# Kernel tuning notes

Measured on AMD Instinct MI355X. Metric: run time of the kernel, lower is better.

## Reference

```python
import jax, jax.numpy as jnp
import numpy as np

N_HEAD = 16
EMBED = 1024
HEAD_DIM = EMBED // N_HEAD  # 64
HALF = HEAD_DIM // 2        # 32
T = 2048                    # total packed tokens
NSEG = 4
SEG = T // NSEG             # 512 tokens per packed sequence
SCALE = HEAD_DIM ** -0.5


def _apply_rotary_vision(t, freqs):
    # t: [T, H, D], freqs: [T, D/2] -> Qwen2-VL style vision RoPE
    cos = jnp.concatenate([jnp.cos(freqs), jnp.cos(freqs)], axis=-1)[:, None, :]  # [T,1,D]
    sin = jnp.concatenate([jnp.sin(freqs), jnp.sin(freqs)], axis=-1)[:, None, :]
    t1, t2 = t[..., :HALF], t[..., HALF:]
    rot = jnp.concatenate([-t2, t1], axis=-1)  # rotate_half
    return t * cos + rot * sin


def setup_inputs() -> dict:
    key = jax.random.key(0)
    k1, k2, k3, k4, k5 = jax.random.split(key, 5)
    hidden_states = jax.random.normal(k1, (T, EMBED), dtype=jnp.float32)
    cu_seqlens = (jnp.arange(NSEG + 1, dtype=jnp.int32) * SEG)  # [0,512,...,2048]
    # realistic rotary freqs: position within each segment * inverse frequencies
    pos = jnp.tile(jnp.arange(SEG, dtype=jnp.float32), NSEG)  # [T]
    inv_freq = 1.0 / (10000.0 ** (jnp.arange(HALF, dtype=jnp.float32) / HALF))
    rotary_pos_emb = pos[:, None] * inv_freq[None, :]  # [T, HALF]
    std = 0.02
    wq = jax.random.normal(k2, (EMBED, EMBED), dtype=jnp.float32) * std
    wk = jax.random.normal(k3, (EMBED, EMBED), dtype=jnp.float32) * std
    wv = jax.random.normal(k4, (EMBED, EMBED), dtype=jnp.float32) * std
    wo = jax.random.normal(k5, (EMBED, EMBED), dtype=jnp.float32) * std
    return {"hidden_states": hidden_states, "cu_seqlens": cu_seqlens,
            "rotary_pos_emb": rotary_pos_emb, "wq": wq, "wk": wk, "wv": wv, "wo": wo}


def reference(hidden_states, cu_seqlens, rotary_pos_emb, wq, wk, wv, wo):
    # QKV projections (nn.Linear, bias=False): y = x @ W.T
    q = (hidden_states @ wq.T).reshape(T, N_HEAD, HEAD_DIM)
    k = (hidden_states @ wk.T).reshape(T, N_HEAD, HEAD_DIM)
    v = (hidden_states @ wv.T).reshape(T, N_HEAD, HEAD_DIM)
    q = _apply_rotary_vision(q, rotary_pos_emb)
    k = _apply_rotary_vision(k, rotary_pos_emb)
    # varlen (block-diagonal, non-causal) attention over packed segments
    seg_id = jnp.searchsorted(cu_seqlens, jnp.arange(T, dtype=cu_seqlens.dtype), side='right')
    same_seg = seg_id[:, None] == seg_id[None, :]  # [T, T]
    scores = jnp.einsum('thd,shd->hts', q, k) * SCALE  # [H, T, T]
    scores = jnp.where(same_seg[None, :, :], scores, jnp.finfo(scores.dtype).min)
    probs = jax.nn.softmax(scores, axis=-1)
    attn = jnp.einsum('hts,shd->thd', probs, v).reshape(T, EMBED)
    return attn @ wo.T
```

## Files before the change

kernel.cpp:

```cpp
#include <hip/hip_runtime.h>
#include <cstdint>

#define T_TOK 2048
#define EMBED 1024
#define NH    16
#define HD    64
#define HALF  32
#define SEG   512
#define SL    (0.125f * 1.44269504088896f)

typedef __attribute__((ext_vector_type(8))) __bf16 bf16x8;
typedef __attribute__((ext_vector_type(4))) float  f32x4;
typedef unsigned short u16;
typedef unsigned int   u32;

__device__ __forceinline__ u16 f2bf(float f) {
  u32 u = __builtin_bit_cast(u32, f);
  u += 0x7fffu + ((u >> 16) & 1u);
  return (u16)(u >> 16);
}

__device__ __forceinline__ void gld_lds16(const void* g, void* l) {
  __builtin_amdgcn_global_load_lds(
      reinterpret_cast<__attribute__((address_space(1))) u32*>(
          reinterpret_cast<uintptr_t>(g)),
      reinterpret_cast<__attribute__((address_space(3))) u32*>(
          reinterpret_cast<uintptr_t>(l)),
      16, 0, 0);
}

__global__ __launch_bounds__(256) void convert_k(
    const float* __restrict__ H,  const float* __restrict__ wq,
    const float* __restrict__ wk, const float* __restrict__ wv,
    const float* __restrict__ wo, u16* __restrict__ dst) {
  const size_t gid = (size_t)blockIdx.x * 256 + threadIdx.x;
  const size_t e = gid * 4;
  const float* src; size_t off;
  const size_t HN = (size_t)T_TOK * EMBED;
  if (e < HN) { src = H; off = e; }
  else {
    size_t r = e - HN;
    int w = (int)(r >> 20);
    off = r & ((1u << 20) - 1);
    src = (w == 0) ? wq : (w == 1) ? wk : (w == 2) ? wv : wo;
  }
  const float4 v = *(const float4*)(src + off);
  ushort4 o;
  o.x = f2bf(v.x); o.y = f2bf(v.y); o.z = f2bf(v.z); o.w = f2bf(v.w);
  *(ushort4*)(dst + e) = o;
}

__global__ __launch_bounds__(256) void qkv_k(
    const u16* __restrict__ Hb, const u16* __restrict__ Wb,
    const float* __restrict__ rope, u16* __restrict__ Qb,
    u16* __restrict__ Khh, u16* __restrict__ Vss) {
  constexpr int K = 1024, N = 1024;
  __shared__ alignas(16) u16 As[2][2][128 * 32];
  __shared__ alignas(16) u16 Bs[2][2][128 * 32];
  const int tid = threadIdx.x;
  const int wave = tid >> 6, lane = tid & 63;
  const int quad = lane >> 4, l16 = lane & 15;
  const int bm = blockIdx.y * 128, bn = blockIdx.x * 128;
  const int z = blockIdx.z;
  const u16* Bz = Wb + ((size_t)z << 20);
  const int wm = (wave >> 1) * 64, wn = (wave & 1) * 64;

  f32x4 acc[4][4];
#pragma unroll
  for (int i = 0; i < 4; ++i)
#pragma unroll
    for (int j = 0; j < 4; ++j) { f32x4 zz = {0.f, 0.f, 0.f, 0.f}; acc[i][j] = zz; }

  const int srow = tid >> 2, scol = (tid & 3) * 8;
  const u16* gA = Hb + (size_t)(bm + srow) * K + scol;
  const u16* gB = Bz + (size_t)(bn + srow) * K + scol;

#pragma unroll
  for (int p = 0; p < 2; ++p)
#pragma unroll
    for (int hrow = 0; hrow < 2; ++hrow) {
      gld_lds16(gA + (size_t)hrow * 64 * K + p * 32,
                (char*)&As[0][p][0] + hrow * 4096 + wave * 1024);
      gld_lds16(gB + (size_t)hrow * 64 * K + p * 32,
                (char*)&Bs[0][p][0] + hrow * 4096 + wave * 1024);
    }

  for (int kk = 0; kk < K; kk += 64) {
    __syncthreads();
    const int cur = (kk >> 6) & 1, nxt = cur ^ 1;
    if (kk + 64 < K) {
      const int kn = kk + 64;
#pragma unroll
      for (int p = 0; p < 2; ++p)
#pragma unroll
        for (int hrow = 0; hrow < 2; ++hrow) {
          gld_lds16(gA + (size_t)hrow * 64 * K + kn + p * 32,
                    (char*)&As[nxt][p][0] + hrow * 4096 + wave * 1024);
          gld_lds16(gB + (size_t)hrow * 64 * K + kn + p * 32,
                    (char*)&Bs[nxt][p][0] + hrow * 4096 + wave * 1024);
        }
    }
#pragma unroll
    for (int p = 0; p < 2; ++p) {
      const u16* Ac = &As[cur][p][0];
      const u16* Bc = &Bs[cur][p][0];
      bf16x8 af[4], bfv[4];
#pragma unroll
      for (int i = 0; i < 4; ++i)
        af[i] = *(const bf16x8*)(Ac + (wm + i * 16 + l16) * 32 + quad * 8);
#pragma unroll
      for (int j = 0; j < 4; ++j)
        bfv[j] = *(const bf16x8*)(Bc + (wn + j * 16 + l16) * 32 + quad * 8);
#pragma unroll
      for (int i = 0; i < 4; ++i)
#pragma unroll
        for (int j = 0; j < 4; ++j)
          acc[i][j] = __builtin_amdgcn_mfma_f32_16x16x32_bf16(af[i], bfv[j],
                                                              acc[i][j], 0, 0, 0);
    }
  }

  const int h = (bn + wn) >> 6;
  if (z == 0) {
#pragma unroll
    for (int i = 0; i < 4; ++i)
#pragma unroll
      for (int r = 0; r < 4; ++r) {
        const int t = bm + wm + i * 16 + quad * 4 + r;
        const float f0 = rope[t * HALF + l16];
        const float f1 = rope[t * HALF + 16 + l16];
        float s0, c0, s1, c1;
        __sincosf(f0, &s0, &c0);
        __sincosf(f1, &s1, &c1);
        const float v0 = acc[i][0][r], v1 = acc[i][1][r];
        const float v2 = acc[i][2][r], v3 = acc[i][3][r];
        const size_t base = (size_t)t * N + bn + wn + l16;
        Qb[base]      = f2bf(v0 * c0 - v2 * s0);
        Qb[base + 16] = f2bf(v1 * c1 - v3 * s1);
        Qb[base + 32] = f2bf(v2 * c0 + v0 * s0);
        Qb[base + 48] = f2bf(v3 * c1 + v1 * s1);
      }
  } else if (z == 1) {
#pragma unroll
    for (int i = 0; i < 4; ++i)
#pragma unroll
      for (int r = 0; r < 4; ++r) {
        const int t = bm + wm + i * 16 + quad * 4 + r;
        const float f0 = rope[t * HALF + l16];
        const float f1 = rope[t * HALF + 16 + l16];
        float s0, c0, s1, c1;
        __sincosf(f0, &s0, &c0);
        __sincosf(f1, &s1, &c1);
        const float v0 = acc[i][0][r], v1 = acc[i][1][r];
        const float v2 = acc[i][2][r], v3 = acc[i][3][r];
        const size_t b0 = ((size_t)(h * 2 + 0) * T_TOK + t) * 32;
        const size_t b1 = ((size_t)(h * 2 + 1) * T_TOK + t) * 32;
        Khh[b0 + l16]      = f2bf(v0 * c0 - v2 * s0);
        Khh[b0 + 16 + l16] = f2bf(v1 * c1 - v3 * s1);
        Khh[b1 + l16]      = f2bf(v2 * c0 + v0 * s0);
        Khh[b1 + 16 + l16] = f2bf(v3 * c1 + v1 * s1);
      }
  } else {
#pragma unroll
    for (int i = 0; i < 4; ++i) {
      const int t0 = bm + wm + i * 16 + quad * 4;
      const int tp = t0 >> 5, toff = t0 & 31;
#pragma unroll
      for (int j = 0; j < 4; ++j) {
        const int d = j * 16 + l16;
        ushort4 pk;
        pk.x = f2bf(acc[i][j][0]); pk.y = f2bf(acc[i][j][1]);
        pk.z = f2bf(acc[i][j][2]); pk.w = f2bf(acc[i][j][3]);
        *(ushort4*)(Vss + ((size_t)(h * 64 + tp) * 64 + d) * 32 + toff) = pk;
      }
    }
  }
}

__global__ __launch_bounds__(512) void attn_st(
    const u16* __restrict__ Qb, const u16* __restrict__ Khh,
    const u16* __restrict__ Vss, u16* __restrict__ Ab) {
  const int b = blockIdx.x;
  const int qt = b & 3, seg = (b >> 2) & 3, h = b >> 4;
  const int tid = threadIdx.x;
  const int wave = tid >> 6, lane = tid & 63;
  const int quad = lane >> 4, l16 = lane & 15;

  __shared__ alignas(16) u16 Ks[2][2][64 * 32];
  __shared__ alignas(16) u16 Vs[2][2][64 * 32];

  const int qbase = seg * SEG + qt * 128 + wave * 16;
  const u16* qp = Qb + (size_t)(qbase + l16) * EMBED + h * HD + quad * 8;
  const bf16x8 qf0 = *(const bf16x8*)qp;
  const bf16x8 qf1 = *(const bf16x8*)(qp + 32);

  const u16* Ksrc0 = Khh + ((size_t)(h * 2 + 0) * T_TOK + seg * SEG) * 32;
  const u16* Ksrc1 = Khh + ((size_t)(h * 2 + 1) * T_TOK + seg * SEG) * 32;
  const u16* Vsrc  = Vss + ((size_t)(h * 64 + seg * 16) * 64) * 32;

  float plsum = 0.f;
  f32x4 O[4];
#pragma unroll
  for (int nt = 0; nt < 4; ++nt) { f32x4 z = {0.f, 0.f, 0.f, 0.f}; O[nt] = z; }

  const int toff = tid * 4;
  const int rb = 8 * (l16 >> 2) + (l16 & 3);

  uint2 kreg0 = *(const uint2*)(Ksrc0 + toff);
  uint2 kreg1 = *(const uint2*)(Ksrc1 + toff);
  uint2 vreg0 = *(const uint2*)(Vsrc + toff);
  uint2 vreg1 = *(const uint2*)(Vsrc + 2048 + toff);
  *(uint2*)((char*)&Ks[0][0][0] + tid * 8) = kreg0;
  *(uint2*)((char*)&Ks[0][1][0] + tid * 8) = kreg1;
  *(uint2*)((char*)&Vs[0][0][0] + tid * 8) = vreg0;
  *(uint2*)((char*)&Vs[0][1][0] + tid * 8) = vreg1;
  kreg0 = *(const uint2*)(Ksrc0 + 2048 + toff);
  kreg1 = *(const uint2*)(Ksrc1 + 2048 + toff);
  vreg0 = *(const uint2*)(Vsrc + 4096 + toff);
  vreg1 = *(const uint2*)(Vsrc + 4096 + 2048 + toff);
  asm volatile("s_waitcnt lgkmcnt(0)" ::: "memory");
  __builtin_amdgcn_s_barrier();
  __builtin_amdgcn_sched_barrier(0);

  int cur = 0;
  for (int cc = 0; cc < 8; ++cc) {
    f32x4 S[4];
    __builtin_amdgcn_s_setprio(1);
#pragma unroll
    for (int kt = 0; kt < 4; ++kt) {
      const int pk = rb + 4 * (kt & 1) + 32 * (kt >> 1);
      const bf16x8 k0 = *(const bf16x8*)&Ks[cur][0][pk * 32 + quad * 8];
      const bf16x8 k1 = *(const bf16x8*)&Ks[cur][1][pk * 32 + quad * 8];
      f32x4 s = {0.f, 0.f, 0.f, 0.f};
      s = __builtin_amdgcn_mfma_f32_16x16x32_bf16(k0, qf0, s, 0, 0, 0);
      s = __builtin_amdgcn_mfma_f32_16x16x32_bf16(k1, qf1, s, 0, 0, 0);
      S[kt] = s;
    }
    __builtin_amdgcn_s_setprio(0);
    bf16x8 vf0[4], vf1[4];
#pragma unroll
    for (int nt = 0; nt < 4; ++nt) {
      vf0[nt] = *(const bf16x8*)&Vs[cur][0][(nt * 16 + l16) * 32 + quad * 8];
      vf1[nt] = *(const bf16x8*)&Vs[cur][1][(nt * 16 + l16) * 32 + quad * 8];
    }
    u32 lo[4], hi[4];
    float plc = 0.f;
#pragma unroll
    for (int kt = 0; kt < 4; ++kt) {
      const float p0 = exp2f(S[kt][0] * SL), p1 = exp2f(S[kt][1] * SL);
      const float p2 = exp2f(S[kt][2] * SL), p3 = exp2f(S[kt][3] * SL);
      plc += (p0 + p1) + (p2 + p3);
      lo[kt] = (u32)f2bf(p0) | ((u32)f2bf(p1) << 16);
      hi[kt] = (u32)f2bf(p2) | ((u32)f2bf(p3) << 16);
    }
    plsum += plc;
    uint4 w0; w0.x = lo[0]; w0.y = hi[0]; w0.z = lo[1]; w0.w = hi[1];
    uint4 w1; w1.x = lo[2]; w1.y = hi[2]; w1.z = lo[3]; w1.w = hi[3];
    const bf16x8 pf0 = __builtin_bit_cast(bf16x8, w0);
    const bf16x8 pf1 = __builtin_bit_cast(bf16x8, w1);
    __builtin_amdgcn_s_setprio(1);
#pragma unroll
    for (int nt = 0; nt < 4; ++nt) {
      O[nt] = __builtin_amdgcn_mfma_f32_16x16x32_bf16(pf0, vf0[nt], O[nt], 0, 0, 0);
      O[nt] = __builtin_amdgcn_mfma_f32_16x16x32_bf16(pf1, vf1[nt], O[nt], 0, 0, 0);
    }
    __builtin_amdgcn_s_setprio(0);
    if (cc < 7) {
      const int nxt = cur ^ 1;
      *(uint2*)((char*)&Ks[nxt][0][0] + tid * 8) = kreg0;
      *(uint2*)((char*)&Ks[nxt][1][0] + tid * 8) = kreg1;
      *(uint2*)((char*)&Vs[nxt][0][0] + tid * 8) = vreg0;
      *(uint2*)((char*)&Vs[nxt][1][0] + tid * 8) = vreg1;
      if (cc < 6) {
        const size_t kc = (size_t)(cc + 2) * 2048 + toff;
        const size_t vc = (size_t)(cc + 2) * 4096 + toff;
        kreg0 = *(const uint2*)(Ksrc0 + kc);
        kreg1 = *(const uint2*)(Ksrc1 + kc);
        vreg0 = *(const uint2*)(Vsrc + vc);
        vreg1 = *(const uint2*)(Vsrc + vc + 2048);
      }
      asm volatile("s_waitcnt lgkmcnt(0)" ::: "memory");
      __builtin_amdgcn_s_barrier();
      __builtin_amdgcn_sched_barrier(0);
    }
    cur ^= 1;
  }
  plsum += __shfl_xor(plsum, 16);
  plsum += __shfl_xor(plsum, 32);
  float inv[4];
#pragma unroll
  for (int r = 0; r < 4; ++r)
    inv[r] = 1.f / __shfl(plsum, quad * 4 + r);
#pragma unroll
  for (int nt = 0; nt < 4; ++nt)
#pragma unroll
    for (int r = 0; r < 4; ++r) {
      const int trow = qbase + quad * 4 + r;
      Ab[(size_t)trow * EMBED + h * HD + nt * 16 + l16] = f2bf(O[nt][r] * inv[r]);
    }
}

__global__ __launch_bounds__(256) void oproj_k(
    const u16* __restrict__ Ab, const u16* __restrict__ Wo,
    float* __restrict__ out) {
  constexpr int K = 1024, N = 1024;
  __shared__ alignas(16) u16 As[2][2][64 * 32];
  __shared__ alignas(16) u16 Bs[2][2][64 * 32];
  const int tid = threadIdx.x;
  const int wave = tid >> 6, lane = tid & 63;
  const int quad = lane >> 4, l16 = lane & 15;
  const int bm = blockIdx.y * 64, bn = blockIdx.x * 64;

  f32x4 acc[4];
#pragma unroll
  for (int j = 0; j < 4; ++j) { f32x4 z = {0.f, 0.f, 0.f, 0.f}; acc[j] = z; }

  const int srow = tid >> 2, scol = (tid & 3) * 8;
  const u16* gA = Ab + (size_t)(bm + srow) * K + scol;
  const u16* gB = Wo + (size_t)(bn + srow) * K + scol;

#pragma unroll
  for (int p = 0; p < 2; ++p) {
    gld_lds16(gA + p * 32, (char*)&As[0][p][0] + wave * 1024);
    gld_lds16(gB + p * 32, (char*)&Bs[0][p][0] + wave * 1024);
  }

  for (int kk = 0; kk < K; kk += 64) {
    __syncthreads();
    const int cur = (kk >> 6) & 1, nxt = cur ^ 1;
    if (kk + 64 < K) {
      const int kn = kk + 64;
#pragma unroll
      for (int p = 0; p < 2; ++p) {
        gld_lds16(gA + kn + p * 32, (char*)&As[nxt][p][0] + wave * 1024);
        gld_lds16(gB + kn + p * 32, (char*)&Bs[nxt][p][0] + wave * 1024);
      }
    }
#pragma unroll
    for (int p = 0; p < 2; ++p) {
      const u16* Ac = &As[cur][p][0];
      const u16* Bc = &Bs[cur][p][0];
      const bf16x8 af = *(const bf16x8*)(Ac + (wave * 16 + l16) * 32 + quad * 8);
      bf16x8 bfv[4];
#pragma unroll
      for (int j = 0; j < 4; ++j)
        bfv[j] = *(const bf16x8*)(Bc + (j * 16 + l16) * 32 + quad * 8);
#pragma unroll
      for (int j = 0; j < 4; ++j)
        acc[j] = __builtin_amdgcn_mfma_f32_16x16x32_bf16(af, bfv[j],
                                                         acc[j], 0, 0, 0);
    }
  }

#pragma unroll
  for (int r = 0; r < 4; ++r) {
    const int row = bm + wave * 16 + quad * 4 + r;
#pragma unroll
    for (int j = 0; j < 4; ++j)
      out[(size_t)row * N + bn + j * 16 + l16] = acc[j][r];
  }
}

extern "C" void kernel_launch(void* const* d_in, const int* in_sizes, int n_in,
                              void* d_out, int out_size, void* d_ws,
                              size_t ws_size, hipStream_t stream) {
  const float* H    = (const float*)d_in[0];
  const float* rope = (const float*)d_in[2];
  const float* wq   = (const float*)d_in[3];
  const float* wk   = (const float*)d_in[4];
  const float* wv   = (const float*)d_in[5];
  const float* wo   = (const float*)d_in[6];
  float* out        = (float*)d_out;

  constexpr size_t M1 = (size_t)1 << 20;
  if (ws_size < 28 * M1) return;

  u16* ws16 = (u16*)d_ws;
  u16* Hb  = ws16;
  u16* Wb  = ws16 + 2 * M1;
  u16* Qb  = ws16 + 6 * M1;
  u16* Khh = ws16 + 8 * M1;
  u16* Vss = ws16 + 10 * M1;
  u16* Ab  = ws16 + 12 * M1;

  convert_k<<<6144, 256, 0, stream>>>(H, wq, wk, wv, wo, ws16);
  qkv_k<<<dim3(8, 16, 3), 256, 0, stream>>>(Hb, Wb, rope, Qb, Khh, Vss);
  attn_st<<<256, 512, 0, stream>>>(Qb, Khh, Vss, Ab);
  oproj_k<<<dim3(16, 32), 256, 0, stream>>>(Ab, Wb + 3 * M1, out);
}
```

Measured before the change: 123.0 us.

## Fuse Q, K, V projections per head into one block sharing the A tile

```diff
diff --git a/kernel.cpp b/kernel.cpp
--- a/kernel.cpp
+++ b/kernel.cpp
@@ -50,129 +50,109 @@
   *(ushort4*)(dst + e) = o;
 }
 
-__global__ __launch_bounds__(256) void qkv_k(
+__global__ __launch_bounds__(512) void qkv_k(
     const u16* __restrict__ Hb, const u16* __restrict__ Wb,
     const float* __restrict__ rope, u16* __restrict__ Qb,
     u16* __restrict__ Khh, u16* __restrict__ Vss) {
-  constexpr int K = 1024, N = 1024;
+  constexpr int K = 1024;
   __shared__ alignas(16) u16 As[2][2][128 * 32];
-  __shared__ alignas(16) u16 Bs[2][2][128 * 32];
+  __shared__ alignas(16) u16 Bs[3][2][2][64 * 32];
   const int tid = threadIdx.x;
   const int wave = tid >> 6, lane = tid & 63;
   const int quad = lane >> 4, l16 = lane & 15;
-  const int bm = blockIdx.y * 128, bn = blockIdx.x * 128;
-  const int z = blockIdx.z;
-  const u16* Bz = Wb + ((size_t)z << 20);
-  const int wm = (wave >> 1) * 64, wn = (wave & 1) * 64;
-
-  f32x4 acc[4][4];
-#pragma unroll
-  for (int i = 0; i < 4; ++i)
-#pragma unroll
-    for (int j = 0; j < 4; ++j) { f32x4 zz = {0.f, 0.f, 0.f, 0.f}; acc[i][j] = zz; }
-
-  const int srow = tid >> 2, scol = (tid & 3) * 8;
-  const u16* gA = Hb + (size_t)(bm + srow) * K + scol;
-  const u16* gB = Bz + (size_t)(bn + srow) * K + scol;
-
-#pragma unroll
-  for (int p = 0; p < 2; ++p)
-#pragma unroll
-    for (int hrow = 0; hrow < 2; ++hrow) {
-      gld_lds16(gA + (size_t)hrow * 64 * K + p * 32,
-                (char*)&As[0][p][0] + hrow * 4096 + wave * 1024);
-      gld_lds16(gB + (size_t)hrow * 64 * K + p * 32,
-                (char*)&Bs[0][p][0] + hrow * 4096 + wave * 1024);
-    }
+  const int h = blockIdx.x, bm = blockIdx.y * 128;
+  const int bn = h * 64;
+  const int wm = (wave >> 1) * 32, ws = wave & 1;
+
+  f32x4 acc[3][2][2];
+#pragma unroll
+  for (int z = 0; z < 3; ++z)
+#pragma unroll
+    for (int i = 0; i < 2; ++i)
+#pragma unroll
+      for (int j = 0; j < 2; ++j) { f32x4 zz = {0.f, 0.f, 0.f, 0.f}; acc[z][i][j] = zz; }
+
+  const u16* gA = Hb + (size_t)(bm + (tid >> 2)) * K + (tid & 3) * 8;
+  const int brow = (tid >> 2) & 63;
+  const int srow = (brow & 15) + ((brow >> 4) & 1) * 32 + (brow >> 5) * 16;
+  const size_t boff = (size_t)(bn + srow) * K + (tid >> 8) * 32 + (tid & 3) * 8;
+  const u16* gB0 = Wb + ((size_t)0 << 20) + boff;
+  const u16* gB1 = Wb + ((size_t)1 << 20) + boff;
+  const u16* gB2 = Wb + ((size_t)2 << 20) + boff;
+
+#define QKV_STAGE(buf, kkk)                                                   \
+  do {                                                                        \
+    gld_lds16(gA + (kkk),      (char*)&As[buf][0][0] + wave * 1024);          \
+    gld_lds16(gA + (kkk) + 32, (char*)&As[buf][1][0] + wave * 1024);          \
+    gld_lds16(gB0 + (kkk), (char*)&Bs[0][buf][0][0] + wave * 1024);           \
+    gld_lds16(gB1 + (kkk), (char*)&Bs[1][buf][0][0] + wave * 1024);           \
+    gld_lds16(gB2 + (kkk), (char*)&Bs[2][buf][0][0] + wave * 1024);           \
+  } while (0)
+
+  QKV_STAGE(0, 0);
 
   for (int kk = 0; kk < K; kk += 64) {
     __syncthreads();
     const int cur = (kk >> 6) & 1, nxt = cur ^ 1;
-    if (kk + 64 < K) {
-      const int kn = kk + 64;
-#pragma unroll
-      for (int p = 0; p < 2; ++p)
-#pragma unroll
-        for (int hrow = 0; hrow < 2; ++hrow) {
-          gld_lds16(gA + (size_t)hrow * 64 * K + kn + p * 32,
-                    (char*)&As[nxt][p][0] + hrow * 4096 + wave * 1024);
-          gld_lds16(gB + (size_t)hrow * 64 * K + kn + p * 32,
-                    (char*)&Bs[nxt][p][0] + hrow * 4096 + wave * 1024);
-        }
-    }
+    if (kk + 64 < K) QKV_STAGE(nxt, kk + 64);
 #pragma unroll
     for (int p = 0; p < 2; ++p) {
-      const u16* Ac = &As[cur][p][0];
-      const u16* Bc = &Bs[cur][p][0];
-      bf16x8 af[4], bfv[4];
-#pragma unroll
-      for (int i = 0; i < 4; ++i)
-        af[i] = *(const bf16x8*)(Ac + (wm + i * 16 + l16) * 32 + quad * 8);
-#pragma unroll
-      for (int j = 0; j < 4; ++j)
-        bfv[j] = *(const bf16x8*)(Bc + (wn + j * 16 + l16) * 32 + quad * 8);
-#pragma unroll
-      for (int i = 0; i < 4; ++i)
-#pragma unroll
-        for (int j = 0; j < 4; ++j)
-          acc[i][j] = __builtin_amdgcn_mfma_f32_16x16x32_bf16(af[i], bfv[j],
-                                                              acc[i][j], 0, 0, 0);
-    }
-  }
-
-  const int h = (bn + wn) >> 6;
-  if (z == 0) {
-#pragma unroll
-    for (int i = 0; i < 4; ++i)
-#pragma unroll
-      for (int r = 0; r < 4; ++r) {
-        const int t = bm + wm + i * 16 + quad * 4 + r;
-        const float f0 = rope[t * HALF + l16];
-        const float f1 = rope[t * HALF + 16 + l16];
-        float s0, c0, s1, c1;
-        __sincosf(f0, &s0, &c0);
-        __sincosf(f1, &s1, &c1);
-        const float v0 = acc[i][0][r], v1 = acc[i][1][r];
-        const float v2 = acc[i][2][r], v3 = acc[i][3][r];
-        const size_t base = (size_t)t * N + bn + wn + l16;
-        Qb[base]      = f2bf(v0 * c0 - v2 * s0);
-        Qb[base + 16] = f2bf(v1 * c1 - v3 * s1);
-        Qb[base + 32] = f2bf(v2 * c0 + v0 * s0);
-        Qb[base + 48] = f2bf(v3 * c1 + v1 * s1);
+      bf16x8 af[2], bfv[3][2];
+#pragma unroll
+      for (int i = 0; i < 2; ++i)
+        af[i] = *(const bf16x8*)(&As[cur][p][0] + (wm + i * 16 + l16) * 32 + quad * 8);
+#pragma unroll
+      for (int z = 0; z < 3; ++z)
+#pragma unroll
+        for (int j = 0; j < 2; ++j)
+          bfv[z][j] = *(const bf16x8*)(&Bs[z][cur][p][0] +
+                                       (ws * 32 + j * 16 + l16) * 32 + quad * 8);
+#pragma unroll
+      for (int z = 0; z < 3; ++z)
+#pragma unroll
+        for (int i = 0; i < 2; ++i)
+#pragma unroll
+          for (int j = 0; j < 2; ++j)
+            acc[z][i][j] = __builtin_amdgcn_mfma_f32_16x16x32_bf16(
+                af[i], bfv[z][j], acc[z][i][j], 0, 0, 0);
+    }
+  }
+#undef QKV_STAGE
+
+  const int dcol = ws * 16 + l16;
+#pragma unroll
+  for (int i = 0; i < 2; ++i)
+#pragma unroll
+    for (int r = 0; r < 4; ++r) {
+      const int t = bm + wm + i * 16 + quad * 4 + r;
+      const float f = rope[t * HALF + dcol];
+      float s, c;
+      __sincosf(f, &s, &c);
+      {
+        const float v0 = acc[0][i][0][r], v1 = acc[0][i][1][r];
+        const size_t base = (size_t)t * EMBED + bn + dcol;
+        Qb[base]      = f2bf(v0 * c - v1 * s);
+        Qb[base + 32] = f2bf(v1 * c + v0 * s);
       }
-  } else if (z == 1) {
-#pragma unroll
-    for (int i = 0; i < 4; ++i)
-#pragma unroll
-      for (int r = 0; r < 4; ++r) {
-        const int t = bm + wm + i * 16 + quad * 4 + r;
-        const float f0 = rope[t * HALF + l16];
-        const float f1 = rope[t * HALF + 16 + l16];
-        float s0, c0, s1, c1;
-        __sincosf(f0, &s0, &c0);
-        __sincosf(f1, &s1, &c1);
-        const float v0 = acc[i][0][r], v1 = acc[i][1][r];
-        const float v2 = acc[i][2][r], v3 = acc[i][3][r];
+      {
+        const float v0 = acc[1][i][0][r], v1 = acc[1][i][1][r];
         const size_t b0 = ((size_t)(h * 2 + 0) * T_TOK + t) * 32;
         const size_t b1 = ((size_t)(h * 2 + 1) * T_TOK + t) * 32;
-        Khh[b0 + l16]      = f2bf(v0 * c0 - v2 * s0);
-        Khh[b0 + 16 + l16] = f2bf(v1 * c1 - v3 * s1);
-        Khh[b1 + l16]      = f2bf(v2 * c0 + v0 * s0);
-        Khh[b1 + 16 + l16] = f2bf(v3 * c1 + v1 * s1);
+        Khh[b0 + dcol] = f2bf(v0 * c - v1 * s);
+        Khh[b1 + dcol] = f2bf(v1 * c + v0 * s);
       }
-  } else {
-#pragma unroll
-    for (int i = 0; i < 4; ++i) {
-      const int t0 = bm + wm + i * 16 + quad * 4;
-      const int tp = t0 >> 5, toff = t0 & 31;
-#pragma unroll
-      for (int j = 0; j < 4; ++j) {
-        const int d = j * 16 + l16;
-        ushort4 pk;
-        pk.x = f2bf(acc[i][j][0]); pk.y = f2bf(acc[i][j][1]);
-        pk.z = f2bf(acc[i][j][2]); pk.w = f2bf(acc[i][j][3]);
-        *(ushort4*)(Vss + ((size_t)(h * 64 + tp) * 64 + d) * 32 + toff) = pk;
-      }
+    }
+#pragma unroll
+  for (int i = 0; i < 2; ++i) {
+    const int t0 = bm + wm + i * 16 + quad * 4;
+    const int tp = t0 >> 5, toff = t0 & 31;
+#pragma unroll
+    for (int j = 0; j < 2; ++j) {
+      const int d = dcol + j * 32;
+      ushort4 pk;
+      pk.x = f2bf(acc[2][i][j][0]); pk.y = f2bf(acc[2][i][j][1]);
+      pk.z = f2bf(acc[2][i][j][2]); pk.w = f2bf(acc[2][i][j][3]);
+      *(ushort4*)(Vss + ((size_t)(h * 64 + tp) * 64 + d) * 32 + toff) = pk;
     }
   }
 }
@@ -384,7 +364,7 @@
   u16* Ab  = ws16 + 12 * M1;
 
   convert_k<<<6144, 256, 0, stream>>>(H, wq, wk, wv, wo, ws16);
-  qkv_k<<<dim3(8, 16, 3), 256, 0, stream>>>(Hb, Wb, rope, Qb, Khh, Vss);
+  qkv_k<<<dim3(16, 16), 512, 0, stream>>>(Hb, Wb, rope, Qb, Khh, Vss);
   attn_st<<<256, 512, 0, stream>>>(Qb, Khh, Vss, Ab);
   oproj_k<<<dim3(16, 32), 256, 0, stream>>>(Ab, Wb + 3 * M1, out);
 }
```

Result: no change. 124.9 us (+1.5%).

## Fuse convert, QKV, attention and out-projection into one cooperative persistent kernel

Applied to the files above, without the earlier changes.

```diff
diff --git a/kernel.cpp b/kernel.cpp
--- a/kernel.cpp
+++ b/kernel.cpp
@@ -1,5 +1,8 @@
 #include <hip/hip_runtime.h>
+#include <hip/hip_cooperative_groups.h>
 #include <cstdint>
+
+namespace cg = cooperative_groups;
 
 #define T_TOK 2048
 #define EMBED 1024
@@ -27,6 +30,329 @@
       reinterpret_cast<__attribute__((address_space(3))) u32*>(
           reinterpret_cast<uintptr_t>(l)),
       16, 0, 0);
+}
+
+#define M1 ((size_t)1 << 20)
+
+__global__ __launch_bounds__(512, 2) void mega_k(
+    const float* __restrict__ H,  const float* __restrict__ wq,
+    const float* __restrict__ wk, const float* __restrict__ wv,
+    const float* __restrict__ wo, const float* __restrict__ rope,
+    u16* __restrict__ ws16, float* __restrict__ out) {
+  cg::grid_group grid = cg::this_grid();
+  __shared__ alignas(16) char smem[81920];
+
+  u16* Hb  = ws16;
+  u16* Wb  = ws16 + 2 * M1;
+  u16* Qb  = ws16 + 6 * M1;
+  u16* Khh = ws16 + 8 * M1;
+  u16* Vss = ws16 + 10 * M1;
+  u16* Ab  = ws16 + 12 * M1;
+  const int tid = threadIdx.x;
+  const int blk = blockIdx.x;
+  const int wave = tid >> 6, lane = tid & 63;
+  const int quad = lane >> 4, l16 = lane & 15;
+
+  {
+    const size_t HN = (size_t)T_TOK * EMBED;
+#pragma unroll
+    for (int it = 0; it < 12; ++it) {
+      const size_t e = ((size_t)(blk * 512 + tid) + (size_t)it * 131072) * 4;
+      const float* src; size_t off;
+      if (e < HN) { src = H; off = e; }
+      else {
+        size_t r = e - HN;
+        int w = (int)(r >> 20);
+        off = r & ((1u << 20) - 1);
+        src = (w == 0) ? wq : (w == 1) ? wk : (w == 2) ? wv : wo;
+      }
+      const float4 v = *(const float4*)(src + off);
+      ushort4 o;
+      o.x = f2bf(v.x); o.y = f2bf(v.y); o.z = f2bf(v.z); o.w = f2bf(v.w);
+      *(ushort4*)(ws16 + e) = o;
+    }
+  }
+  __threadfence();
+  grid.sync();
+
+  {
+    auto As = reinterpret_cast<u16 (*)[2][128 * 32]>(smem);
+    auto Bs = reinterpret_cast<u16 (*)[2][2][64 * 32]>(smem + 32768);
+    constexpr int K = 1024;
+    const int h = blk & 15, bm = (blk >> 4) * 128;
+    const int bn = h * 64;
+    const int wm = (wave >> 1) * 32, ws = wave & 1;
+
+    f32x4 acc[3][2][2];
+#pragma unroll
+    for (int z = 0; z < 3; ++z)
+#pragma unroll
+      for (int i = 0; i < 2; ++i)
+#pragma unroll
+        for (int j = 0; j < 2; ++j) { f32x4 zz = {0.f, 0.f, 0.f, 0.f}; acc[z][i][j] = zz; }
+
+    const u16* gA = Hb + (size_t)(bm + (tid >> 2)) * K + (tid & 3) * 8;
+    const int brow = (tid >> 2) & 63;
+    const int srow = (brow & 15) + ((brow >> 4) & 1) * 32 + (brow >> 5) * 16;
+    const size_t boff = (size_t)(bn + srow) * K + (tid >> 8) * 32 + (tid & 3) * 8;
+    const u16* gB0 = Wb + ((size_t)0 << 20) + boff;
+    const u16* gB1 = Wb + ((size_t)1 << 20) + boff;
+    const u16* gB2 = Wb + ((size_t)2 << 20) + boff;
+
+#define QKV_STAGE(buf, kkk)                                                   \
+  do {                                                                        \
+    gld_lds16(gA + (kkk),      (char*)&As[buf][0][0] + wave * 1024);          \
+    gld_lds16(gA + (kkk) + 32, (char*)&As[buf][1][0] + wave * 1024);          \
+    gld_lds16(gB0 + (kkk), (char*)&Bs[0][buf][0][0] + wave * 1024);           \
+    gld_lds16(gB1 + (kkk), (char*)&Bs[1][buf][0][0] + wave * 1024);           \
+    gld_lds16(gB2 + (kkk), (char*)&Bs[2][buf][0][0] + wave * 1024);           \
+  } while (0)
+
+    QKV_STAGE(0, 0);
+
+    for (int kk = 0; kk < K; kk += 64) {
+      __syncthreads();
+      const int cur = (kk >> 6) & 1, nxt = cur ^ 1;
+      if (kk + 64 < K) QKV_STAGE(nxt, kk + 64);
+#pragma unroll
+      for (int p = 0; p < 2; ++p) {
+        bf16x8 af[2], bfv[3][2];
+#pragma unroll
+        for (int i = 0; i < 2; ++i)
+          af[i] = *(const bf16x8*)(&As[cur][p][0] + (wm + i * 16 + l16) * 32 + quad * 8);
+#pragma unroll
+        for (int z = 0; z < 3; ++z)
+#pragma unroll
+          for (int j = 0; j < 2; ++j)
+            bfv[z][j] = *(const bf16x8*)(&Bs[z][cur][p][0] +
+                                         (ws * 32 + j * 16 + l16) * 32 + quad * 8);
+#pragma unroll
+        for (int z = 0; z < 3; ++z)
+#pragma unroll
+          for (int i = 0; i < 2; ++i)
+#pragma unroll
+            for (int j = 0; j < 2; ++j)
+              acc[z][i][j] = __builtin_amdgcn_mfma_f32_16x16x32_bf16(
+                  af[i], bfv[z][j], acc[z][i][j], 0, 0, 0);
+      }
+    }
+#undef QKV_STAGE
+
+    const int dcol = ws * 16 + l16;
+#pragma unroll
+    for (int i = 0; i < 2; ++i)
+#pragma unroll
+      for (int r = 0; r < 4; ++r) {
+        const int t = bm + wm + i * 16 + quad * 4 + r;
+        const float f = rope[t * HALF + dcol];
+        float s, c;
+        __sincosf(f, &s, &c);
+        {
+          const float v0 = acc[0][i][0][r], v1 = acc[0][i][1][r];
+          const size_t base = (size_t)t * EMBED + bn + dcol;
+          Qb[base]      = f2bf(v0 * c - v1 * s);
+          Qb[base + 32] = f2bf(v1 * c + v0 * s);
+        }
+        {
+          const float v0 = acc[1][i][0][r], v1 = acc[1][i][1][r];
+          const size_t b0 = ((size_t)(h * 2 + 0) * T_TOK + t) * 32;
+          const size_t b1 = ((size_t)(h * 2 + 1) * T_TOK + t) * 32;
+          Khh[b0 + dcol] = f2bf(v0 * c - v1 * s);
+          Khh[b1 + dcol] = f2bf(v1 * c + v0 * s);
+        }
+      }
+#pragma unroll
+    for (int i = 0; i < 2; ++i) {
+      const int t0 = bm + wm + i * 16 + quad * 4;
+      const int tp = t0 >> 5, toff = t0 & 31;
+#pragma unroll
+      for (int j = 0; j < 2; ++j) {
+        const int d = dcol + j * 32;
+        ushort4 pk;
+        pk.x = f2bf(acc[2][i][j][0]); pk.y = f2bf(acc[2][i][j][1]);
+        pk.z = f2bf(acc[2][i][j][2]); pk.w = f2bf(acc[2][i][j][3]);
+        *(ushort4*)(Vss + ((size_t)(h * 64 + tp) * 64 + d) * 32 + toff) = pk;
+      }
+    }
+  }
+  __threadfence();
+  grid.sync();
+
+  {
+    auto Ks = reinterpret_cast<u16 (*)[2][64 * 32]>(smem);
+    auto Vs = reinterpret_cast<u16 (*)[2][64 * 32]>(smem + 16384);
+    const int qt = blk & 3, seg = (blk >> 2) & 3, h = blk >> 4;
+
+    const int qbase = seg * SEG + qt * 128 + wave * 16;
+    const u16* qp = Qb + (size_t)(qbase + l16) * EMBED + h * HD + quad * 8;
+    const bf16x8 qf0 = *(const bf16x8*)qp;
+    const bf16x8 qf1 = *(const bf16x8*)(qp + 32);
+
+    const u16* Ksrc0 = Khh + ((size_t)(h * 2 + 0) * T_TOK + seg * SEG) * 32;
+    const u16* Ksrc1 = Khh + ((size_t)(h * 2 + 1) * T_TOK + seg * SEG) * 32;
+    const u16* Vsrc  = Vss + ((size_t)(h * 64 + seg * 16) * 64) * 32;
+
+    float plsum = 0.f;
+    f32x4 O[4];
+#pragma unroll
+    for (int nt = 0; nt < 4; ++nt) { f32x4 z = {0.f, 0.f, 0.f, 0.f}; O[nt] = z; }
+
+    const int toff = tid * 4;
+    const int rb = 8 * (l16 >> 2) + (l16 & 3);
+
+    uint2 kreg0 = *(const uint2*)(Ksrc0 + toff);
+    uint2 kreg1 = *(const uint2*)(Ksrc1 + toff);
+    uint2 vreg0 = *(const uint2*)(Vsrc + toff);
+    uint2 vreg1 = *(const uint2*)(Vsrc + 2048 + toff);
+    *(uint2*)((char*)&Ks[0][0][0] + tid * 8) = kreg0;
+    *(uint2*)((char*)&Ks[0][1][0] + tid * 8) = kreg1;
+    *(uint2*)((char*)&Vs[0][0][0] + tid * 8) = vreg0;
+    *(uint2*)((char*)&Vs[0][1][0] + tid * 8) = vreg1;
+    kreg0 = *(const uint2*)(Ksrc0 + 2048 + toff);
+    kreg1 = *(const uint2*)(Ksrc1 + 2048 + toff);
+    vreg0 = *(const uint2*)(Vsrc + 4096 + toff);
+    vreg1 = *(const uint2*)(Vsrc + 4096 + 2048 + toff);
+    asm volatile("s_waitcnt lgkmcnt(0)" ::: "memory");
+    __builtin_amdgcn_s_barrier();
+    __builtin_amdgcn_sched_barrier(0);
+
+    int cur = 0;
+    for (int cc = 0; cc < 8; ++cc) {
+      f32x4 S[4];
+      __builtin_amdgcn_s_setprio(1);
+#pragma unroll
+      for (int kt = 0; kt < 4; ++kt) {
+        const int pk = rb + 4 * (kt & 1) + 32 * (kt >> 1);
+        const bf16x8 k0 = *(const bf16x8*)&Ks[cur][0][pk * 32 + quad * 8];
+        const bf16x8 k1 = *(const bf16x8*)&Ks[cur][1][pk * 32 + quad * 8];
+        f32x4 s = {0.f, 0.f, 0.f, 0.f};
+        s = __builtin_amdgcn_mfma_f32_16x16x32_bf16(k0, qf0, s, 0, 0, 0);
+        s = __builtin_amdgcn_mfma_f32_16x16x32_bf16(k1, qf1, s, 0, 0, 0);
+        S[kt] = s;
+      }
+      __builtin_amdgcn_s_setprio(0);
+      bf16x8 vf0[4], vf1[4];
+#pragma unroll
+      for (int nt = 0; nt < 4; ++nt) {
+        vf0[nt] = *(const bf16x8*)&Vs[cur][0][(nt * 16 + l16) * 32 + quad * 8];
+        vf1[nt] = *(const bf16x8*)&Vs[cur][1][(nt * 16 + l16) * 32 + quad * 8];
+      }
+      u32 lo[4], hi[4];
+      float plc = 0.f;
+#pragma unroll
+      for (int kt = 0; kt < 4; ++kt) {
+        const float p0 = exp2f(S[kt][0] * SL), p1 = exp2f(S[kt][1] * SL);
+        const float p2 = exp2f(S[kt][2] * SL), p3 = exp2f(S[kt][3] * SL);
+        plc += (p0 + p1) + (p2 + p3);
+        lo[kt] = (u32)f2bf(p0) | ((u32)f2bf(p1) << 16);
+        hi[kt] = (u32)f2bf(p2) | ((u32)f2bf(p3) << 16);
+      }
+      plsum += plc;
+      uint4 w0; w0.x = lo[0]; w0.y = hi[0]; w0.z = lo[1]; w0.w = hi[1];
+      uint4 w1; w1.x = lo[2]; w1.y = hi[2]; w1.z = lo[3]; w1.w = hi[3];
+      const bf16x8 pf0 = __builtin_bit_cast(bf16x8, w0);
+      const bf16x8 pf1 = __builtin_bit_cast(bf16x8, w1);
+      __builtin_amdgcn_s_setprio(1);
+#pragma unroll
+      for (int nt = 0; nt < 4; ++nt) {
+        O[nt] = __builtin_amdgcn_mfma_f32_16x16x32_bf16(pf0, vf0[nt], O[nt], 0, 0, 0);
+        O[nt] = __builtin_amdgcn_mfma_f32_16x16x32_bf16(pf1, vf1[nt], O[nt], 0, 0, 0);
+      }
+      __builtin_amdgcn_s_setprio(0);
+      if (cc < 7) {
+        const int nxt = cur ^ 1;
+        *(uint2*)((char*)&Ks[nxt][0][0] + tid * 8) = kreg0;
+        *(uint2*)((char*)&Ks[nxt][1][0] + tid * 8) = kreg1;
+        *(uint2*)((char*)&Vs[nxt][0][0] + tid * 8) = vreg0;
+        *(uint2*)((char*)&Vs[nxt][1][0] + tid * 8) = vreg1;
+        if (cc < 6) {
+          const size_t kc = (size_t)(cc + 2) * 2048 + toff;
+          const size_t vc = (size_t)(cc + 2) * 4096 + toff;
+          kreg0 = *(const uint2*)(Ksrc0 + kc);
+          kreg1 = *(const uint2*)(Ksrc1 + kc);
+          vreg0 = *(const uint2*)(Vsrc + vc);
+          vreg1 = *(const uint2*)(Vsrc + vc + 2048);
+        }
+        asm volatile("s_waitcnt lgkmcnt(0)" ::: "memory");
+        __builtin_amdgcn_s_barrier();
+        __builtin_amdgcn_sched_barrier(0);
+      }
+      cur ^= 1;
+    }
+    plsum += __shfl_xor(plsum, 16);
+    plsum += __shfl_xor(plsum, 32);
+    float inv[4];
+#pragma unroll
+    for (int r = 0; r < 4; ++r)
+      inv[r] = 1.f / __shfl(plsum, quad * 4 + r);
+#pragma unroll
+    for (int nt = 0; nt < 4; ++nt)
+#pragma unroll
+      for (int r = 0; r < 4; ++r) {
+        const int trow = qbase + quad * 4 + r;
+        Ab[(size_t)trow * EMBED + h * HD + nt * 16 + l16] = f2bf(O[nt][r] * inv[r]);
+      }
+  }
+  __threadfence();
+  grid.sync();
+
+  {
+    auto As2 = reinterpret_cast<u16 (*)[2][2][64 * 32]>(smem);
+    auto Bs2 = reinterpret_cast<u16 (*)[2][2][64 * 32]>(smem + 32768);
+    const u16* Wo16 = Wb + 3 * M1;
+    const int h2 = wave >> 2, wl = wave & 3;
+    const int vb = blk * 2 + h2;
+    const int bn = (vb & 15) * 64, bm = (vb >> 4) * 64;
+    const int l2 = tid & 255;
+
+    f32x4 acc[4];
+#pragma unroll
+    for (int j = 0; j < 4; ++j) { f32x4 z = {0.f, 0.f, 0.f, 0.f}; acc[j] = z; }
+
+    const int srow = l2 >> 2, scol = (l2 & 3) * 8;
+    const u16* gA = Ab + (size_t)(bm + srow) * 1024 + scol;
+    const u16* gB = Wo16 + (size_t)(bn + srow) * 1024 + scol;
+
+#pragma unroll
+    for (int p = 0; p < 2; ++p) {
+      gld_lds16(gA + p * 32, (char*)&As2[h2][0][p][0] + wl * 1024);
+      gld_lds16(gB + p * 32, (char*)&Bs2[h2][0][p][0] + wl * 1024);
+    }
+
+    for (int kk = 0; kk < 1024; kk += 64) {
+      __syncthreads();
+      const int cur = (kk >> 6) & 1, nxt = cur ^ 1;
+      if (kk + 64 < 1024) {
+        const int kn = kk + 64;
+#pragma unroll
+        for (int p = 0; p < 2; ++p) {
+          gld_lds16(gA + kn + p * 32, (char*)&As2[h2][nxt][p][0] + wl * 1024);
+          gld_lds16(gB + kn + p * 32, (char*)&Bs2[h2][nxt][p][0] + wl * 1024);
+        }
+      }
+#pragma unroll
+      for (int p = 0; p < 2; ++p) {
+        const u16* Ac = &As2[h2][cur][p][0];
+        const u16* Bc = &Bs2[h2][cur][p][0];
+        const bf16x8 af = *(const bf16x8*)(Ac + (wl * 16 + l16) * 32 + quad * 8);
+        bf16x8 bfv[4];
+#pragma unroll
+        for (int j = 0; j < 4; ++j)
+          bfv[j] = *(const bf16x8*)(Bc + (j * 16 + l16) * 32 + quad * 8);
+#pragma unroll
+        for (int j = 0; j < 4; ++j)
+          acc[j] = __builtin_amdgcn_mfma_f32_16x16x32_bf16(af, bfv[j],
+                                                           acc[j], 0, 0, 0);
+      }
+    }
+#pragma unroll
+    for (int r = 0; r < 4; ++r) {
+      const int row = bm + wl * 16 + quad * 4 + r;
+#pragma unroll
+      for (int j = 0; j < 4; ++j)
+        out[(size_t)row * 1024 + bn + j * 16 + l16] = acc[j][r];
+    }
+  }
 }
 
 __global__ __launch_bounds__(256) void convert_k(
@@ -372,19 +698,24 @@
   const float* wo   = (const float*)d_in[6];
   float* out        = (float*)d_out;
 
-  constexpr size_t M1 = (size_t)1 << 20;
   if (ws_size < 28 * M1) return;
 
   u16* ws16 = (u16*)d_ws;
-  u16* Hb  = ws16;
-  u16* Wb  = ws16 + 2 * M1;
-  u16* Qb  = ws16 + 6 * M1;
-  u16* Khh = ws16 + 8 * M1;
-  u16* Vss = ws16 + 10 * M1;
-  u16* Ab  = ws16 + 12 * M1;
-
-  convert_k<<<6144, 256, 0, stream>>>(H, wq, wk, wv, wo, ws16);
-  qkv_k<<<dim3(8, 16, 3), 256, 0, stream>>>(Hb, Wb, rope, Qb, Khh, Vss);
-  attn_st<<<256, 512, 0, stream>>>(Qb, Khh, Vss, Ab);
-  oproj_k<<<dim3(16, 32), 256, 0, stream>>>(Ab, Wb + 3 * M1, out);
+
+  void* kargs[] = {(void*)&H, (void*)&wq, (void*)&wk, (void*)&wv, (void*)&wo,
+                   (void*)&rope, (void*)&ws16, (void*)&out};
+  hipError_t ce = hipLaunchCooperativeKernel(
+      reinterpret_cast<void*>(mega_k), dim3(256), dim3(512), kargs, 0, stream);
+  if (ce != hipSuccess) {
+    u16* Hb  = ws16;
+    u16* Wb  = ws16 + 2 * M1;
+    u16* Qb  = ws16 + 6 * M1;
+    u16* Khh = ws16 + 8 * M1;
+    u16* Vss = ws16 + 10 * M1;
+    u16* Ab  = ws16 + 12 * M1;
+    convert_k<<<6144, 256, 0, stream>>>(H, wq, wk, wv, wo, ws16);
+    qkv_k<<<dim3(8, 16, 3), 256, 0, stream>>>(Hb, Wb, rope, Qb, Khh, Vss);
+    attn_st<<<256, 512, 0, stream>>>(Qb, Khh, Vss, Ab);
+    oproj_k<<<dim3(16, 32), 256, 0, stream>>>(Ab, Wb + 3 * M1, out);
+  }
 }
```

New measurement: 403.5 us. 228% more time.

## Fuse fp32-to-bf16 conversion into GEMM tile loads and drop convert kernel

Applied to the files above, without the earlier changes.

```diff
diff --git a/kernel.cpp b/kernel.cpp
--- a/kernel.cpp
+++ b/kernel.cpp
@@ -29,29 +29,18 @@
       16, 0, 0);
 }
 
-__global__ __launch_bounds__(256) void convert_k(
-    const float* __restrict__ H,  const float* __restrict__ wq,
-    const float* __restrict__ wk, const float* __restrict__ wv,
-    const float* __restrict__ wo, u16* __restrict__ dst) {
-  const size_t gid = (size_t)blockIdx.x * 256 + threadIdx.x;
-  const size_t e = gid * 4;
-  const float* src; size_t off;
-  const size_t HN = (size_t)T_TOK * EMBED;
-  if (e < HN) { src = H; off = e; }
-  else {
-    size_t r = e - HN;
-    int w = (int)(r >> 20);
-    off = r & ((1u << 20) - 1);
-    src = (w == 0) ? wq : (w == 1) ? wk : (w == 2) ? wv : wo;
-  }
-  const float4 v = *(const float4*)(src + off);
-  ushort4 o;
-  o.x = f2bf(v.x); o.y = f2bf(v.y); o.z = f2bf(v.z); o.w = f2bf(v.w);
-  *(ushort4*)(dst + e) = o;
+__device__ __forceinline__ void cvt_write(const float4* s, void* dst) {
+  bf16x8 o;
+  o[0] = (__bf16)s[0].x; o[1] = (__bf16)s[0].y;
+  o[2] = (__bf16)s[0].z; o[3] = (__bf16)s[0].w;
+  o[4] = (__bf16)s[1].x; o[5] = (__bf16)s[1].y;
+  o[6] = (__bf16)s[1].z; o[7] = (__bf16)s[1].w;
+  *(bf16x8*)dst = o;
 }
 
 __global__ __launch_bounds__(256) void qkv_k(
-    const u16* __restrict__ Hb, const u16* __restrict__ Wb,
+    const float* __restrict__ Hf, const float* __restrict__ wqf,
+    const float* __restrict__ wkf, const float* __restrict__ wvf,
     const float* __restrict__ rope, u16* __restrict__ Qb,
     u16* __restrict__ Khh, u16* __restrict__ Vss) {
   constexpr int K = 1024, N = 1024;
@@ -62,7 +51,7 @@
   const int quad = lane >> 4, l16 = lane & 15;
   const int bm = blockIdx.y * 128, bn = blockIdx.x * 128;
   const int z = blockIdx.z;
-  const u16* Bz = Wb + ((size_t)z << 20);
+  const float* Bzf = (z == 0) ? wqf : (z == 1) ? wkf : wvf;
   const int wm = (wave >> 1) * 64, wn = (wave & 1) * 64;
 
   f32x4 acc[4][4];
@@ -72,34 +61,46 @@
     for (int j = 0; j < 4; ++j) { f32x4 zz = {0.f, 0.f, 0.f, 0.f}; acc[i][j] = zz; }
 
   const int srow = tid >> 2, scol = (tid & 3) * 8;
-  const u16* gA = Hb + (size_t)(bm + srow) * K + scol;
-  const u16* gB = Bz + (size_t)(bn + srow) * K + scol;
-
-#pragma unroll
-  for (int p = 0; p < 2; ++p)
-#pragma unroll
-    for (int hrow = 0; hrow < 2; ++hrow) {
-      gld_lds16(gA + (size_t)hrow * 64 * K + p * 32,
-                (char*)&As[0][p][0] + hrow * 4096 + wave * 1024);
-      gld_lds16(gB + (size_t)hrow * 64 * K + p * 32,
-                (char*)&Bs[0][p][0] + hrow * 4096 + wave * 1024);
-    }
+  const float* gA = Hf  + (size_t)(bm + srow) * K + scol;
+  const float* gB = Bzf + (size_t)(bn + srow) * K + scol;
+
+  float4 sa[4][2], sb[4][2];
+
+#define QKV_LOAD(kn)                                                          \
+  do {                                                                        \
+    _Pragma("unroll")                                                         \
+    for (int p_ = 0; p_ < 2; ++p_)                                            \
+      _Pragma("unroll")                                                       \
+      for (int hr_ = 0; hr_ < 2; ++hr_) {                                     \
+        const float* pa_ = gA + (size_t)hr_ * 64 * K + (kn) + p_ * 32;        \
+        const float* pb_ = gB + (size_t)hr_ * 64 * K + (kn) + p_ * 32;        \
+        sa[p_ * 2 + hr_][0] = *(const float4*)pa_;                            \
+        sa[p_ * 2 + hr_][1] = *(const float4*)(pa_ + 4);                      \
+        sb[p_ * 2 + hr_][0] = *(const float4*)pb_;                            \
+        sb[p_ * 2 + hr_][1] = *(const float4*)(pb_ + 4);                      \
+      }                                                                       \
+  } while (0)
+
+#define QKV_WRITE(buf)                                                        \
+  do {                                                                        \
+    _Pragma("unroll")                                                         \
+    for (int p_ = 0; p_ < 2; ++p_)                                            \
+      _Pragma("unroll")                                                       \
+      for (int hr_ = 0; hr_ < 2; ++hr_) {                                     \
+        cvt_write(sa[p_ * 2 + hr_],                                           \
+                  (char*)&As[buf][p_][0] + hr_ * 4096 + wave * 1024 + lane * 16); \
+        cvt_write(sb[p_ * 2 + hr_],                                           \
+                  (char*)&Bs[buf][p_][0] + hr_ * 4096 + wave * 1024 + lane * 16); \
+      }                                                                       \
+  } while (0)
+
+  QKV_LOAD(0);
+  QKV_WRITE(0);
 
   for (int kk = 0; kk < K; kk += 64) {
     __syncthreads();
     const int cur = (kk >> 6) & 1, nxt = cur ^ 1;
-    if (kk + 64 < K) {
-      const int kn = kk + 64;
-#pragma unroll
-      for (int p = 0; p < 2; ++p)
-#pragma unroll
-        for (int hrow = 0; hrow < 2; ++hrow) {
-          gld_lds16(gA + (size_t)hrow * 64 * K + kn + p * 32,
-                    (char*)&As[nxt][p][0] + hrow * 4096 + wave * 1024);
-          gld_lds16(gB + (size_t)hrow * 64 * K + kn + p * 32,
-                    (char*)&Bs[nxt][p][0] + hrow * 4096 + wave * 1024);
-        }
-    }
+    if (kk + 64 < K) QKV_LOAD(kk + 64);
 #pragma unroll
     for (int p = 0; p < 2; ++p) {
       const u16* Ac = &As[cur][p][0];
@@ -118,7 +119,10 @@
           acc[i][j] = __builtin_amdgcn_mfma_f32_16x16x32_bf16(af[i], bfv[j],
                                                               acc[i][j], 0, 0, 0);
     }
+    if (kk + 64 < K) QKV_WRITE(nxt);
   }
+#undef QKV_LOAD
+#undef QKV_WRITE
 
   const int h = (bn + wn) >> 6;
   if (z == 0) {
@@ -301,7 +305,7 @@
 }
 
 __global__ __launch_bounds__(256) void oproj_k(
-    const u16* __restrict__ Ab, const u16* __restrict__ Wo,
+    const u16* __restrict__ Ab, const float* __restrict__ Wof,
     float* __restrict__ out) {
   constexpr int K = 1024, N = 1024;
   __shared__ alignas(16) u16 As[2][2][64 * 32];
@@ -316,14 +320,34 @@
   for (int j = 0; j < 4; ++j) { f32x4 z = {0.f, 0.f, 0.f, 0.f}; acc[j] = z; }
 
   const int srow = tid >> 2, scol = (tid & 3) * 8;
-  const u16* gA = Ab + (size_t)(bm + srow) * K + scol;
-  const u16* gB = Wo + (size_t)(bn + srow) * K + scol;
-
-#pragma unroll
-  for (int p = 0; p < 2; ++p) {
+  const u16*   gA = Ab  + (size_t)(bm + srow) * K + scol;
+  const float* gB = Wof + (size_t)(bn + srow) * K + scol;
+
+  float4 sbo[2][2];
+
+#define OP_LOADB(kn)                                                          \
+  do {                                                                        \
+    _Pragma("unroll")                                                         \
+    for (int p_ = 0; p_ < 2; ++p_) {                                          \
+      const float* pb_ = gB + (kn) + p_ * 32;                                 \
+      sbo[p_][0] = *(const float4*)pb_;                                       \
+      sbo[p_][1] = *(const float4*)(pb_ + 4);                                 \
+    }                                                                         \
+  } while (0)
+
+#define OP_WRITEB(buf)                                                        \
+  do {                                                                        \
+    _Pragma("unroll")                                                         \
+    for (int p_ = 0; p_ < 2; ++p_)                                            \
+      cvt_write(sbo[p_],                                                      \
+                (char*)&Bs[buf][p_][0] + wave * 1024 + lane * 16);            \
+  } while (0)
+
+  OP_LOADB(0);
+  OP_WRITEB(0);
+#pragma unroll
+  for (int p = 0; p < 2; ++p)
     gld_lds16(gA + p * 32, (char*)&As[0][p][0] + wave * 1024);
-    gld_lds16(gB + p * 32, (char*)&Bs[0][p][0] + wave * 1024);
-  }
 
   for (int kk = 0; kk < K; kk += 64) {
     __syncthreads();
@@ -331,10 +355,9 @@
     if (kk + 64 < K) {
       const int kn = kk + 64;
 #pragma unroll
-      for (int p = 0; p < 2; ++p) {
+      for (int p = 0; p < 2; ++p)
         gld_lds16(gA + kn + p * 32, (char*)&As[nxt][p][0] + wave * 1024);
-        gld_lds16(gB + kn + p * 32, (char*)&Bs[nxt][p][0] + wave * 1024);
-      }
+      OP_LOADB(kn);
     }
 #pragma unroll
     for (int p = 0; p < 2; ++p) {
@@ -350,7 +373,10 @@
         acc[j] = __builtin_amdgcn_mfma_f32_16x16x32_bf16(af, bfv[j],
                                                          acc[j], 0, 0, 0);
     }
+    if (kk + 64 < K) OP_WRITEB(nxt);
   }
+#undef OP_LOADB
+#undef OP_WRITEB
 
 #pragma unroll
   for (int r = 0; r < 4; ++r) {
@@ -376,15 +402,12 @@
   if (ws_size < 28 * M1) return;
 
   u16* ws16 = (u16*)d_ws;
-  u16* Hb  = ws16;
-  u16* Wb  = ws16 + 2 * M1;
   u16* Qb  = ws16 + 6 * M1;
   u16* Khh = ws16 + 8 * M1;
   u16* Vss = ws16 + 10 * M1;
   u16* Ab  = ws16 + 12 * M1;
 
-  convert_k<<<6144, 256, 0, stream>>>(H, wq, wk, wv, wo, ws16);
-  qkv_k<<<dim3(8, 16, 3), 256, 0, stream>>>(Hb, Wb, rope, Qb, Khh, Vss);
+  qkv_k<<<dim3(8, 16, 3), 256, 0, stream>>>(H, wq, wk, wv, rope, Qb, Khh, Vss);
   attn_st<<<256, 512, 0, stream>>>(Qb, Khh, Vss, Ab);
-  oproj_k<<<dim3(16, 32), 256, 0, stream>>>(Ab, Wb + 3 * M1, out);
-}
+  oproj_k<<<dim3(16, 32), 256, 0, stream>>>(Ab, wo, out);
+}
```

Result: slower. 132.3 us (+7.6%).
